# Kernel tuning notes

Measured on AMD Instinct MI355X. Metric: run time of the kernel, lower is better.

## Reference

```python
import jax, jax.numpy as jnp
import numpy as np

N = 3072        # seeds = 3 * batch (src, dst, neg)
K = 64          # num_tokens (sampled neighbors per seed)
C = 128         # edge_dim (mixer channels)
T = 100         # time_dim
ND = 128        # node_dim
ED = 128        # embed_dim
NUM_NODES = 100000
TG = 98304      # total flattened time-gap neighbor indices
L = 2           # num mixer layers
TH = int(K * 0.5)   # token hidden = 32
CH = int(C * 4.0)   # channel hidden = 512
PAD = 0         # PADDED_NODE_ID


def setup_inputs() -> dict:
    key = jax.random.key(0)
    ks = jax.random.split(key, 32)
    inp = {}
    inp['edge_feat'] = jax.random.normal(ks[0], (N, K, C), jnp.float32)
    inp['seed_times'] = jax.random.uniform(ks[1], (N,), jnp.float32) * 1000.0
    inp['nbr_time'] = jax.random.uniform(ks[2], (N, K), jnp.float32) * 1000.0
    inp['node_feat'] = jax.random.normal(ks[3], (NUM_NODES, ND), jnp.float32)
    # Time2Vec frozen frequencies (GraphMixer style)
    inp['time_w'] = jnp.asarray(1.0 / np.power(10.0, np.linspace(0.0, 9.0, T)), jnp.float32)
    s = 0.02
    inp['proj_W'] = jax.random.normal(ks[4], (C + T, C), jnp.float32) * s
    inp['proj_b'] = jnp.zeros((C,), jnp.float32)
    inp['ln1_g'] = jnp.ones((L, C), jnp.float32)
    inp['ln1_b'] = jnp.zeros((L, C), jnp.float32)
    inp['tW1'] = jax.random.normal(ks[5], (L, K, TH), jnp.float32) * s
    inp['tb1'] = jnp.zeros((L, TH), jnp.float32)
    inp['tW2'] = jax.random.normal(ks[6], (L, TH, K), jnp.float32) * s
    inp['tb2'] = jnp.zeros((L, K), jnp.float32)
    inp['ln2_g'] = jnp.ones((L, C), jnp.float32)
    inp['ln2_b'] = jnp.zeros((L, C), jnp.float32)
    inp['cW1'] = jax.random.normal(ks[7], (L, C, CH), jnp.float32) * s
    inp['cb1'] = jnp.zeros((L, CH), jnp.float32)
    inp['cW2'] = jax.random.normal(ks[8], (L, CH, C), jnp.float32) * s
    inp['cb2'] = jnp.zeros((L, C), jnp.float32)
    inp['out_W'] = jax.random.normal(ks[9], (C + ND, ED), jnp.float32) * s
    inp['out_b'] = jnp.zeros((ED,), jnp.float32)
    inp['nbr_nids'] = jax.random.randint(ks[10], (N, K), 0, NUM_NODES, jnp.int32)
    inp['tg_idx'] = jax.random.randint(ks[11], (TG,), 0, NUM_NODES, jnp.int32)
    inp['tg_seg'] = jnp.sort(jax.random.randint(ks[12], (TG,), 0, N, jnp.int32))
    inp['seed_ids'] = jax.random.randint(ks[13], (N,), 0, NUM_NODES, jnp.int32)
    return inp


def _ln(x, g, b):
    m = jnp.mean(x, axis=-1, keepdims=True)
    v = jnp.var(x, axis=-1, keepdims=True)
    return (x - m) * jax.lax.rsqrt(v + 1e-5) * g + b


def reference(edge_feat, seed_times, nbr_time, node_feat, time_w, proj_W, proj_b,
              ln1_g, ln1_b, tW1, tb1, tW2, tb2, ln2_g, ln2_b, cW1, cb1, cW2, cb2,
              out_W, out_b, nbr_nids, tg_idx, tg_seg, seed_ids):
    # Time2Vec on time deltas: [N, K, T]
    dt = seed_times[:, None] - nbr_time
    tfeat = jnp.cos(dt[..., None] * time_w)
    # projection: [N, K, C]
    z = jnp.concatenate([edge_feat, tfeat], axis=-1) @ proj_W + proj_b
    # MLP-Mixer layers (token mixing over K, channel mixing over C)
    for l in range(L):
        h = _ln(z, ln1_g[l], ln1_b[l])
        h = jnp.einsum('nkc,kh->nhc', h, tW1[l]) + tb1[l][None, :, None]
        h = jax.nn.gelu(h)
        h = jnp.einsum('nhc,hk->nkc', h, tW2[l]) + tb2[l][None, :, None]
        z = z + h
        h = _ln(z, ln2_g[l], ln2_b[l])
        h = jax.nn.gelu(h @ cW1[l] + cb1[l]) @ cW2[l] + cb2[l]
        z = z + h
    # masked mean over valid neighbors -> [N, C]
    mask = (nbr_nids != PAD).astype(z.dtype)
    z = jnp.sum(z * mask[..., None], axis=1) / jnp.clip(jnp.sum(mask, axis=1, keepdims=True), 1.0)
    # ragged segment-mean over time-gap neighbors (replaces Python loop)
    counts = jax.ops.segment_sum(jnp.ones((TG,), z.dtype), tg_seg, num_segments=N)
    tg_feat = jax.ops.segment_sum(node_feat[tg_idx], tg_seg, num_segments=N) / jnp.clip(counts, 1.0)[:, None]
    z_node = tg_feat + node_feat[seed_ids]
    return jnp.concatenate([z, z_node], axis=1) @ out_W + out_b
```

## Files before the change

### kernel.cpp

```cpp
#include <hip/hip_runtime.h>
#include <math.h>

#define NS   3072
#define KT   64
#define CC   128
#define TDIM 100
#define TGN  98304
#define TH   32
#define CH   512
#define ZS   132
#define PS   136
#define PS2  264
#define PSK  72
#define PSH  40

typedef __attribute__((ext_vector_type(8))) short bf16x8;
typedef __attribute__((ext_vector_type(4))) float f32x4;

__device__ __forceinline__ unsigned short f2bf(float f) {
    unsigned int u = __float_as_uint(f);
    return (unsigned short)((u + 0x7FFFu + ((u >> 16) & 1u)) >> 16);
}
__device__ __forceinline__ float fast_exp2(float x) {
    float r; asm("v_exp_f32 %0, %1" : "=v"(r) : "v"(x)); return r;
}
__device__ __forceinline__ float fast_rcp(float x) {
    float r; asm("v_rcp_f32 %0, %1" : "=v"(r) : "v"(x)); return r;
}
__device__ __forceinline__ float fast_cos2pi(float rev) {
    float f = rev - floorf(rev);
    float r; asm("v_cos_f32 %0, %1" : "=v"(r) : "v"(f)); return r;
}
__device__ __forceinline__ unsigned int pk_bf16(float lo, float hi) {
    unsigned int r; asm("v_cvt_pk_bf16_f32 %0, %1, %2" : "=v"(r) : "v"(lo), "v"(hi)); return r;
}
__device__ __forceinline__ float gelu_f(float x) {
    float p = x * x;
    float e = fast_exp2(-x * fmaf(p, 0.1029436f, 2.3022082f));
    return x * fast_rcp(1.0f + e);
}

__global__ void gm_prep(const float* __restrict__ proj_W, const float* __restrict__ tW1,
                        const float* __restrict__ tW2, const float* __restrict__ cW1,
                        const float* __restrict__ cW2,
                        unsigned short* __restrict__ projWTb, unsigned short* __restrict__ tW1Tb,
                        unsigned short* __restrict__ tW2Tb, unsigned short* __restrict__ cW1Tb,
                        unsigned short* __restrict__ cW2Tb)
{
    int e = blockIdx.x * 256 + threadIdx.x;
    if (e < 32768) {
        int c = e >> 8, j = e & 255;
        projWTb[e] = (j < 228) ? f2bf(proj_W[j * CC + c]) : (unsigned short)0;
    }
    int e1 = e - 32768;
    if (e1 >= 0 && e1 < 4096) {
        int l = e1 >> 11, rem = e1 & 2047, h = rem >> 6, k = rem & 63;
        tW1Tb[e1] = f2bf(tW1[(l * KT + k) * TH + h]);
    }
    int e2 = e - 36864;
    if (e2 >= 0 && e2 < 4096) {
        int l = e2 >> 11, rem = e2 & 2047, k = rem >> 5, h = rem & 31;
        tW2Tb[e2] = f2bf(tW2[(l * TH + h) * KT + k]);
    }
    int e3 = e - 40960;
    if (e3 >= 0 && e3 < 131072) {
        int l = e3 >> 16, rem = e3 & 65535, h = rem >> 7, c = rem & 127;
        cW1Tb[e3] = f2bf(cW1[(l * CC + c) * CH + h]);
    }
    int e4 = e - 172032;
    if (e4 >= 0 && e4 < 131072) {
        int l = e4 >> 16, rem = e4 & 65535, c = rem >> 9, h = rem & 511;
        cW2Tb[e4] = f2bf(cW2[(l * CH + h) * CC + c]);
    }
}

__global__ __launch_bounds__(256, 2)
void gm_mixer(const float* __restrict__ edge_feat,
              const float* __restrict__ seed_times,
              const float* __restrict__ nbr_time,
              const float* __restrict__ time_w,
              const float* __restrict__ proj_b,
              const float* __restrict__ ln1_g, const float* __restrict__ ln1_b,
              const float* __restrict__ tb1,   const float* __restrict__ tb2,
              const float* __restrict__ ln2_g, const float* __restrict__ ln2_b,
              const float* __restrict__ cb1,   const float* __restrict__ cb2,
              const int*   __restrict__ nbr_nids,
              const unsigned short* __restrict__ projWTb,
              const unsigned short* __restrict__ tW1Tb,
              const unsigned short* __restrict__ tW2Tb,
              const unsigned short* __restrict__ cW1Tb,
              const unsigned short* __restrict__ cW2Tb,
              float* __restrict__ zmean)
{
    __shared__ float zbuf[KT * ZS];
    __shared__ short ubuf[17408];
    __shared__ float mArr[KT], rArr[KT], maskArr[KT];

    const int n  = blockIdx.x;
    const int t  = threadIdx.x;
    const int w  = t >> 6;
    const int l  = t & 63;
    const int lr = l & 15;
    const int kg = l >> 4;

    const f32x4 zero4 = {0.f, 0.f, 0.f, 0.f};

    short* Ab = ubuf;
    if (t < KT) {
        mArr[t]    = seed_times[n] - nbr_time[n * KT + t];
        maskArr[t] = (nbr_nids[n * KT + t] != 0) ? 1.0f : 0.0f;
    }
    {
        const float4* ef4 = (const float4*)(edge_feat + (size_t)n * KT * CC);
        #pragma unroll
        for (int it = 0; it < 8; ++it) {
            int i4 = it * 256 + t;
            int k  = i4 >> 5;
            int c  = (i4 & 31) << 2;
            float4 v = ef4[i4];
            uint2 pk;
            pk.x = pk_bf16(v.x, v.y);
            pk.y = pk_bf16(v.z, v.w);
            *(uint2*)&Ab[k * PS2 + c] = pk;
        }
    }
    __syncthreads();
    for (int idx = t; idx < 4096; idx += 256) {
        int k = idx >> 6, j2 = (idx & 63) << 1;
        unsigned int pack = 0;
        if (j2 < TDIM) {
            float dt = mArr[k];
            float2 twv = *(const float2*)&time_w[j2];
            float v0 = fast_cos2pi(dt * twv.x * 0.15915494309f);
            float v1 = fast_cos2pi(dt * twv.y * 0.15915494309f);
            pack = pk_bf16(v0, v1);
        }
        *(unsigned int*)&Ab[k * PS2 + 128 + j2] = pack;
    }
    __syncthreads();

    {
        f32x4 acc[4][2];
        #pragma unroll
        for (int mt = 0; mt < 4; ++mt) { acc[mt][0] = zero4; acc[mt][1] = zero4; }
        for (int ks = 0; ks < 8; ++ks) {
            bf16x8 b0 = *(const bf16x8*)&projWTb[(w * 32 + lr)      * 256 + ks * 32 + kg * 8];
            bf16x8 b1 = *(const bf16x8*)&projWTb[(w * 32 + 16 + lr) * 256 + ks * 32 + kg * 8];
            #pragma unroll
            for (int mt = 0; mt < 4; ++mt) {
                bf16x8 a = *(const bf16x8*)&Ab[(mt * 16 + lr) * PS2 + ks * 32 + kg * 8];
                acc[mt][0] = __builtin_amdgcn_mfma_f32_16x16x32_bf16(a, b0, acc[mt][0], 0, 0, 0);
                acc[mt][1] = __builtin_amdgcn_mfma_f32_16x16x32_bf16(a, b1, acc[mt][1], 0, 0, 0);
            }
        }
        __syncthreads();
        #pragma unroll
        for (int mt = 0; mt < 4; ++mt)
            #pragma unroll
            for (int nt = 0; nt < 2; ++nt) {
                int col = w * 32 + nt * 16 + lr;
                float pb = proj_b[col];
                #pragma unroll
                for (int r = 0; r < 4; ++r)
                    zbuf[(mt * 16 + kg * 4 + r) * ZS + col] = acc[mt][nt][r] + pb;
            }
    }
    __syncthreads();

    short* LNz1T = ubuf;
    short* G2T   = ubuf + 128 * PSK;
    short* LNzb  = ubuf;
    short* Gb    = ubuf + 64 * PS;

    for (int lay = 0; lay < 2; ++lay) {
        {
            int rr = t >> 2, part = t & 3;
            const float4* zp = (const float4*)&zbuf[rr * ZS + part * 32];
            float s = 0.f, s2 = 0.f;
            #pragma unroll
            for (int i = 0; i < 8; ++i) {
                float4 v = zp[i];
                s  += v.x + v.y + v.z + v.w;
                s2 += v.x * v.x + v.y * v.y + v.z * v.z + v.w * v.w;
            }
            s += __shfl_xor(s, 1); s2 += __shfl_xor(s2, 1);
            s += __shfl_xor(s, 2); s2 += __shfl_xor(s2, 2);
            if (part == 0) {
                float m = s * (1.0f / CC);
                float var = s2 * (1.0f / CC) - m * m;
                mArr[rr] = m; rArr[rr] = rsqrtf(var + 1e-5f);
            }
        }
        __syncthreads();

        {
            const float* g1 = ln1_g + lay * CC;
            const float* b1 = ln1_b + lay * CC;
            const int kk = l;
            const float mk = mArr[kk], rk = rArr[kk];
            #pragma unroll
            for (int it = 0; it < 16; ++it) {
                int c = w * 2 + it * 8;
                float2 zv = *(const float2*)&zbuf[kk * ZS + c];
                float v0 = (zv.x - mk) * rk * g1[c]     + b1[c];
                float v1 = (zv.y - mk) * rk * g1[c + 1] + b1[c + 1];
                unsigned int pk = pk_bf16(v0, v1);
                LNz1T[c * PSK + kk]       = (short)(pk & 0xFFFFu);
                LNz1T[(c + 1) * PSK + kk] = (short)(pk >> 16);
            }
        }
        __syncthreads();

        {
            f32x4 acc1[2][2];
            #pragma unroll
            for (int mt = 0; mt < 2; ++mt) { acc1[mt][0] = zero4; acc1[mt][1] = zero4; }
            #pragma unroll
            for (int ks = 0; ks < 2; ++ks) {
                bf16x8 bb0 = *(const bf16x8*)&LNz1T[(w * 32 + lr)      * PSK + ks * 32 + kg * 8];
                bf16x8 bb1 = *(const bf16x8*)&LNz1T[(w * 32 + 16 + lr) * PSK + ks * 32 + kg * 8];
                #pragma unroll
                for (int mt = 0; mt < 2; ++mt) {
                    bf16x8 a = *(const bf16x8*)&tW1Tb[lay * 2048 + (mt * 16 + lr) * 64 + ks * 32 + kg * 8];
                    acc1[mt][0] = __builtin_amdgcn_mfma_f32_16x16x32_bf16(a, bb0, acc1[mt][0], 0, 0, 0);
                    acc1[mt][1] = __builtin_amdgcn_mfma_f32_16x16x32_bf16(a, bb1, acc1[mt][1], 0, 0, 0);
                }
            }
            #pragma unroll
            for (int mt = 0; mt < 2; ++mt) {
                float4 tbv = *(const float4*)&tb1[lay * TH + mt * 16 + kg * 4];
                #pragma unroll
                for (int nt = 0; nt < 2; ++nt) {
                    int col = w * 32 + nt * 16 + lr;
                    float g0 = gelu_f(acc1[mt][nt][0] + tbv.x);
                    float g1v = gelu_f(acc1[mt][nt][1] + tbv.y);
                    float g2 = gelu_f(acc1[mt][nt][2] + tbv.z);
                    float g3 = gelu_f(acc1[mt][nt][3] + tbv.w);
                    uint2 pk;
                    pk.x = pk_bf16(g0, g1v);
                    pk.y = pk_bf16(g2, g3);
                    *(uint2*)&G2T[col * PSH + mt * 16 + kg * 4] = pk;
                }
            }
        }
        {
            f32x4 acc2[4][2];
            #pragma unroll
            for (int mt = 0; mt < 4; ++mt) { acc2[mt][0] = zero4; acc2[mt][1] = zero4; }
            bf16x8 bb0 = *(const bf16x8*)&G2T[(w * 32 + lr)      * PSH + kg * 8];
            bf16x8 bb1 = *(const bf16x8*)&G2T[(w * 32 + 16 + lr) * PSH + kg * 8];
            #pragma unroll
            for (int mt = 0; mt < 4; ++mt) {
                bf16x8 a = *(const bf16x8*)&tW2Tb[lay * 2048 + (mt * 16 + lr) * 32 + kg * 8];
                acc2[mt][0] = __builtin_amdgcn_mfma_f32_16x16x32_bf16(a, bb0, acc2[mt][0], 0, 0, 0);
                acc2[mt][1] = __builtin_amdgcn_mfma_f32_16x16x32_bf16(a, bb1, acc2[mt][1], 0, 0, 0);
            }
            #pragma unroll
            for (int mt = 0; mt < 4; ++mt)
                #pragma unroll
                for (int nt = 0; nt < 2; ++nt) {
                    int col = w * 32 + nt * 16 + lr;
                    #pragma unroll
                    for (int r = 0; r < 4; ++r) {
                        int row = mt * 16 + kg * 4 + r;
                        zbuf[row * ZS + col] += acc2[mt][nt][r] + tb2[lay * KT + row];
                    }
                }
        }
        __syncthreads();

        {
            int rr = t >> 2, part = t & 3;
            const float4* zp = (const float4*)&zbuf[rr * ZS + part * 32];
            float s = 0.f, s2 = 0.f;
            #pragma unroll
            for (int i = 0; i < 8; ++i) {
                float4 v = zp[i];
                s  += v.x + v.y + v.z + v.w;
                s2 += v.x * v.x + v.y * v.y + v.z * v.z + v.w * v.w;
            }
            s += __shfl_xor(s, 1); s2 += __shfl_xor(s2, 1);
            s += __shfl_xor(s, 2); s2 += __shfl_xor(s2, 2);
            if (part == 0) {
                float m = s * (1.0f / CC);
                float var = s2 * (1.0f / CC) - m * m;
                mArr[rr] = m; rArr[rr] = rsqrtf(var + 1e-5f);
            }
        }
        __syncthreads();

        {
            const float* g2 = ln2_g + lay * CC;
            const float* b2 = ln2_b + lay * CC;
            for (int idx = t; idx < 4096; idx += 256) {
                int k = idx >> 6, c2 = (idx & 63) << 1;
                float m = mArr[k], r = rArr[k];
                float v0 = (zbuf[k * ZS + c2]     - m) * r * g2[c2]     + b2[c2];
                float v1 = (zbuf[k * ZS + c2 + 1] - m) * r * g2[c2 + 1] + b2[c2 + 1];
                *(unsigned int*)&LNzb[k * PS + c2] = pk_bf16(v0, v1);
            }
        }
        __syncthreads();

        {
            f32x4 accB[4][2];
            #pragma unroll
            for (int mt = 0; mt < 4; ++mt) { accB[mt][0] = zero4; accB[mt][1] = zero4; }

            for (int jc = 0; jc < 4; ++jc) {
                f32x4 accA[4][2];
                #pragma unroll
                for (int mt = 0; mt < 4; ++mt) { accA[mt][0] = zero4; accA[mt][1] = zero4; }
                #pragma unroll
                for (int ks = 0; ks < 4; ++ks) {
                    const unsigned short* w1p = cW1Tb + lay * CH * CC
                                              + (jc * 128 + w * 32 + lr) * CC + ks * 32 + kg * 8;
                    bf16x8 a0 = *(const bf16x8*)w1p;
                    bf16x8 a1 = *(const bf16x8*)(w1p + 16 * CC);
                    #pragma unroll
                    for (int mt = 0; mt < 4; ++mt) {
                        bf16x8 b = *(const bf16x8*)&LNzb[(mt * 16 + lr) * PS + ks * 32 + kg * 8];
                        accA[mt][0] = __builtin_amdgcn_mfma_f32_16x16x32_bf16(a0, b, accA[mt][0], 0, 0, 0);
                        accA[mt][1] = __builtin_amdgcn_mfma_f32_16x16x32_bf16(a1, b, accA[mt][1], 0, 0, 0);
                    }
                }
                #pragma unroll
                for (int nt = 0; nt < 2; ++nt) {
                    int j0 = w * 32 + nt * 16 + kg * 4;
                    float4 cbv = *(const float4*)&cb1[lay * CH + jc * 128 + j0];
                    #pragma unroll
                    for (int mt = 0; mt < 4; ++mt) {
                        float g0 = gelu_f(accA[mt][nt][0] + cbv.x);
                        float g1v = gelu_f(accA[mt][nt][1] + cbv.y);
                        float g2 = gelu_f(accA[mt][nt][2] + cbv.z);
                        float g3 = gelu_f(accA[mt][nt][3] + cbv.w);
                        uint2 pk;
                        pk.x = pk_bf16(g0, g1v);
                        pk.y = pk_bf16(g2, g3);
                        *(uint2*)&Gb[(mt * 16 + lr) * PS + j0] = pk;
                    }
                }
                __syncthreads();
                #pragma unroll
                for (int ks = 0; ks < 4; ++ks) {
                    const unsigned short* w2p = cW2Tb + lay * CC * CH
                                              + (w * 32 + lr) * CH + jc * 128 + ks * 32 + kg * 8;
                    bf16x8 b0 = *(const bf16x8*)w2p;
                    bf16x8 b1 = *(const bf16x8*)(w2p + 16 * CH);
                    #pragma unroll
                    for (int mt = 0; mt < 4; ++mt) {
                        bf16x8 a = *(const bf16x8*)&Gb[(mt * 16 + lr) * PS + ks * 32 + kg * 8];
                        accB[mt][0] = __builtin_amdgcn_mfma_f32_16x16x32_bf16(a, b0, accB[mt][0], 0, 0, 0);
                        accB[mt][1] = __builtin_amdgcn_mfma_f32_16x16x32_bf16(a, b1, accB[mt][1], 0, 0, 0);
                    }
                }
                __syncthreads();
            }
            #pragma unroll
            for (int mt = 0; mt < 4; ++mt)
                #pragma unroll
                for (int nt = 0; nt < 2; ++nt) {
                    int col = w * 32 + nt * 16 + lr;
                    float cb = cb2[lay * CC + col];
                    #pragma unroll
                    for (int r = 0; r < 4; ++r)
                        zbuf[(mt * 16 + kg * 4 + r) * ZS + col] += accB[mt][nt][r] + cb;
                }
        }
        __syncthreads();
    }

    {
        float* red = (float*)ubuf;
        const int c = t & 127, h = t >> 7;
        float acc = 0.f, ms = 0.f;
        for (int k = h * 32; k < h * 32 + 32; ++k) {
            float mk = maskArr[k];
            ms  += mk;
            acc += zbuf[k * ZS + c] * mk;
        }
        red[h * 128 + c] = acc;
        red[256 + h * 128 + c] = ms;
        __syncthreads();
        if (t < CC) {
            float tot  = red[t] + red[128 + t];
            float mtot = red[256 + t] + red[384 + t];
            zmean[n * CC + t] = tot / fmaxf(mtot, 1.0f);
        }
    }
}

__global__ __launch_bounds__(256)
void gm_out(const float* __restrict__ zmean,
            const float* __restrict__ node_feat,
            const float* __restrict__ out_W,
            const float* __restrict__ out_b,
            const int*   __restrict__ tg_idx,
            const int*   __restrict__ tg_seg,
            const int*   __restrict__ seed_ids,
            float* __restrict__ outp)
{
    __shared__ float redf[8 * 132];
    __shared__ float zmL[CC], znL[CC], oL[2 * CC];
    const int n = blockIdx.x;
    const int t = threadIdx.x;
    const int q = t & 31, g = t >> 5;

    int a = 0, b = TGN;
    while (a < b) { int mm = (a + b) >> 1; if (tg_seg[mm] < n) a = mm + 1; else b = mm; }
    const int lo = a;
    int a2 = lo, b2 = TGN;
    while (a2 < b2) { int mm = (a2 + b2) >> 1; if (tg_seg[mm] < n + 1) a2 = mm + 1; else b2 = mm; }
    const int hi = a2;

    float4 acc = {0.f, 0.f, 0.f, 0.f};
    for (int i = lo + g; i < hi; i += 8) {
        int nid = tg_idx[i];
        const float4* nf = (const float4*)(node_feat + (size_t)nid * CC);
        float4 v = nf[q];
        acc.x += v.x; acc.y += v.y; acc.z += v.z; acc.w += v.w;
    }
    *(float4*)&redf[g * 132 + q * 4] = acc;
    __syncthreads();
    if (t < CC) {
        float s = 0.f;
        #pragma unroll
        for (int gg = 0; gg < 8; ++gg) s += redf[gg * 132 + t];
        float cnt = (float)(hi - lo);
        znL[t] = s / fmaxf(cnt, 1.0f) + node_feat[(size_t)seed_ids[n] * CC + t];
        zmL[t] = zmean[n * CC + t];
    }
    __syncthreads();
    {
        const int c = t & 127, h = t >> 7;
        const float* src = h ? znL : zmL;
        const float* Wp  = out_W + (size_t)h * CC * 128;
        float o = 0.f;
        for (int j = 0; j < CC; ++j) o += src[j] * Wp[j * 128 + c];
        oL[h * 128 + c] = o;
    }
    __syncthreads();
    if (t < CC) outp[n * 128 + t] = oL[t] + oL[CC + t] + out_b[t];
}

extern "C" void kernel_launch(void* const* d_in, const int* in_sizes, int n_in,
                              void* d_out, int out_size, void* d_ws, size_t ws_size,
                              hipStream_t stream)
{
    const float* edge_feat  = (const float*)d_in[0];
    const float* seed_times = (const float*)d_in[1];
    const float* nbr_time   = (const float*)d_in[2];
    const float* node_feat  = (const float*)d_in[3];
    const float* time_w     = (const float*)d_in[4];
    const float* proj_W     = (const float*)d_in[5];
    const float* proj_b     = (const float*)d_in[6];
    const float* ln1_g      = (const float*)d_in[7];
    const float* ln1_b      = (const float*)d_in[8];
    const float* tW1        = (const float*)d_in[9];
    const float* tb1        = (const float*)d_in[10];
    const float* tW2        = (const float*)d_in[11];
    const float* tb2        = (const float*)d_in[12];
    const float* ln2_g      = (const float*)d_in[13];
    const float* ln2_b      = (const float*)d_in[14];
    const float* cW1        = (const float*)d_in[15];
    const float* cb1        = (const float*)d_in[16];
    const float* cW2        = (const float*)d_in[17];
    const float* cb2        = (const float*)d_in[18];
    const float* out_W      = (const float*)d_in[19];
    const float* out_b      = (const float*)d_in[20];
    const int*   nbr_nids   = (const int*)d_in[21];
    const int*   tg_idx     = (const int*)d_in[22];
    const int*   tg_seg     = (const int*)d_in[23];
    const int*   seed_ids   = (const int*)d_in[24];

    char* ws = (char*)d_ws;
    float*          zmean   = (float*)ws;
    unsigned short* projWTb = (unsigned short*)(ws + 1572864);
    unsigned short* tW1Tb   = (unsigned short*)(ws + 1638400);
    unsigned short* tW2Tb   = (unsigned short*)(ws + 1646592);
    unsigned short* cW1Tb   = (unsigned short*)(ws + 1654784);
    unsigned short* cW2Tb   = (unsigned short*)(ws + 1916928);

    gm_prep<<<1184, 256, 0, stream>>>(proj_W, tW1, tW2, cW1, cW2,
                                      projWTb, tW1Tb, tW2Tb, cW1Tb, cW2Tb);
    gm_mixer<<<NS, 256, 0, stream>>>(edge_feat, seed_times, nbr_time, time_w,
                                     proj_b, ln1_g, ln1_b, tb1, tb2, ln2_g, ln2_b,
                                     cb1, cb2, nbr_nids,
                                     projWTb, tW1Tb, tW2Tb, cW1Tb, cW2Tb, zmean);
    gm_out<<<NS, 256, 0, stream>>>(zmean, node_feat, out_W, out_b,
                                   tg_idx, tg_seg, seed_ids, (float*)d_out);
}
```

Baseline: 571.0 us.

## Keep mixer residual stream in registers and drop fp32 LDS z buffer

The residual activation z now stays in MFMA accumulator registers across both mixer layers instead of an fp32 shared-memory buffer. LayerNorm statistics come from cross-lane shuffles plus a small per-wave partial-sum array, and the masked mean reduces in registers. With the large LDS buffer gone, the launch bound rises to three blocks per CU, and the projection GEMM is split into two passes so the time features reuse the edge-feature staging area. Weight preparation becomes tiled LDS transposes for coalesced access; more live registers may cause spills under the tighter occupancy bound.

```diff
diff --git a/kernel.cpp b/kernel.cpp
--- a/kernel.cpp
+++ b/kernel.cpp
@@ -8,9 +8,8 @@
 #define TGN  98304
 #define TH   32
 #define CH   512
-#define ZS   132
 #define PS   136
-#define PS2  264
+#define PSA  136
 #define PSK  72
 #define PSH  40
 
@@ -40,41 +39,57 @@
     return x * fast_rcp(1.0f + e);
 }
 
-__global__ void gm_prep(const float* __restrict__ proj_W, const float* __restrict__ tW1,
-                        const float* __restrict__ tW2, const float* __restrict__ cW1,
-                        const float* __restrict__ cW2,
-                        unsigned short* __restrict__ projWTb, unsigned short* __restrict__ tW1Tb,
-                        unsigned short* __restrict__ tW2Tb, unsigned short* __restrict__ cW1Tb,
-                        unsigned short* __restrict__ cW2Tb)
+__global__ __launch_bounds__(256)
+void gm_trans(const float* __restrict__ cW1, const float* __restrict__ cW2,
+              const float* __restrict__ proj_W,
+              unsigned short* __restrict__ cW1Tb, unsigned short* __restrict__ cW2Tb,
+              unsigned short* __restrict__ projWTb)
+{
+    __shared__ float tile[32][33];
+    const int bid = blockIdx.x;
+    const float* src; unsigned short* dst;
+    int R, Cs, oC, tr, tc;
+    if (bid < 128) {
+        int l = bid >> 6, q = bid & 63; tr = q >> 4; tc = q & 15;
+        src = cW1 + l * CC * CH; dst = cW1Tb + l * CH * CC; R = CC; Cs = CH; oC = CC;
+    } else if (bid < 256) {
+        int b = bid - 128, l = b >> 6, q = b & 63; tr = q & 15; tc = q >> 4;
+        src = cW2 + l * CH * CC; dst = cW2Tb + l * CC * CH; R = CH; Cs = CC; oC = CH;
+    } else {
+        int b = bid - 256; tr = b >> 2; tc = b & 3;
+        src = proj_W; dst = projWTb; R = 228; Cs = CC; oC = 256;
+    }
+    const int tx = threadIdx.x & 31, ty0 = threadIdx.x >> 5;
+    #pragma unroll
+    for (int i = 0; i < 4; ++i) {
+        int ty = ty0 + i * 8;
+        int rr = tr * 32 + ty, cc = tc * 32 + tx;
+        tile[ty][tx] = (rr < R) ? src[rr * Cs + cc] : 0.0f;
+    }
+    __syncthreads();
+    #pragma unroll
+    for (int i = 0; i < 4; ++i) {
+        int ty = ty0 + i * 8;
+        int orow = tc * 32 + ty, ocol = tr * 32 + tx;
+        dst[orow * oC + ocol] = f2bf(tile[tx][ty]);
+    }
+}
+
+__global__ __launch_bounds__(256)
+void gm_prep_small(const float* __restrict__ tW1, const float* __restrict__ tW2,
+                   unsigned short* __restrict__ tW1Tb, unsigned short* __restrict__ tW2Tb)
 {
     int e = blockIdx.x * 256 + threadIdx.x;
-    if (e < 32768) {
-        int c = e >> 8, j = e & 255;
-        projWTb[e] = (j < 228) ? f2bf(proj_W[j * CC + c]) : (unsigned short)0;
-    }
-    int e1 = e - 32768;
-    if (e1 >= 0 && e1 < 4096) {
-        int l = e1 >> 11, rem = e1 & 2047, h = rem >> 6, k = rem & 63;
-        tW1Tb[e1] = f2bf(tW1[(l * KT + k) * TH + h]);
-    }
-    int e2 = e - 36864;
-    if (e2 >= 0 && e2 < 4096) {
-        int l = e2 >> 11, rem = e2 & 2047, k = rem >> 5, h = rem & 31;
+    if (e < 4096) {
+        int l = e >> 11, rem = e & 2047, h = rem >> 6, k = rem & 63;
+        tW1Tb[e] = f2bf(tW1[(l * KT + k) * TH + h]);
+    } else {
+        int e2 = e - 4096, l = e2 >> 11, rem = e2 & 2047, k = rem >> 5, h = rem & 31;
         tW2Tb[e2] = f2bf(tW2[(l * TH + h) * KT + k]);
     }
-    int e3 = e - 40960;
-    if (e3 >= 0 && e3 < 131072) {
-        int l = e3 >> 16, rem = e3 & 65535, h = rem >> 7, c = rem & 127;
-        cW1Tb[e3] = f2bf(cW1[(l * CC + c) * CH + h]);
-    }
-    int e4 = e - 172032;
-    if (e4 >= 0 && e4 < 131072) {
-        int l = e4 >> 16, rem = e4 & 65535, c = rem >> 9, h = rem & 511;
-        cW2Tb[e4] = f2bf(cW2[(l * CH + h) * CC + c]);
-    }
-}
-
-__global__ __launch_bounds__(256, 2)
+}
+
+__global__ __launch_bounds__(256, 3)
 void gm_mixer(const float* __restrict__ edge_feat,
               const float* __restrict__ seed_times,
               const float* __restrict__ nbr_time,
@@ -92,9 +107,9 @@
               const unsigned short* __restrict__ cW2Tb,
               float* __restrict__ zmean)
 {
-    __shared__ float zbuf[KT * ZS];
     __shared__ short ubuf[17408];
-    __shared__ float mArr[KT], rArr[KT], maskArr[KT];
+    __shared__ float lnS[256], lnS2[256];
+    __shared__ float mArr[KT], rArr[KT], maskArr[KT], dtArr[KT];
 
     const int n  = blockIdx.x;
     const int t  = threadIdx.x;
@@ -102,114 +117,134 @@
     const int l  = t & 63;
     const int lr = l & 15;
     const int kg = l >> 4;
-
-    const f32x4 zero4 = {0.f, 0.f, 0.f, 0.f};
-
-    short* Ab = ubuf;
-    if (t < KT) {
-        mArr[t]    = seed_times[n] - nbr_time[n * KT + t];
-        maskArr[t] = (nbr_nids[n * KT + t] != 0) ? 1.0f : 0.0f;
-    }
-    {
-        const float4* ef4 = (const float4*)(edge_feat + (size_t)n * KT * CC);
-        #pragma unroll
-        for (int it = 0; it < 8; ++it) {
-            int i4 = it * 256 + t;
-            int k  = i4 >> 5;
-            int c  = (i4 & 31) << 2;
-            float4 v = ef4[i4];
-            uint2 pk;
-            pk.x = pk_bf16(v.x, v.y);
-            pk.y = pk_bf16(v.z, v.w);
-            *(uint2*)&Ab[k * PS2 + c] = pk;
-        }
-    }
-    __syncthreads();
-    for (int idx = t; idx < 4096; idx += 256) {
-        int k = idx >> 6, j2 = (idx & 63) << 1;
-        unsigned int pack = 0;
-        if (j2 < TDIM) {
-            float dt = mArr[k];
-            float2 twv = *(const float2*)&time_w[j2];
-            float v0 = fast_cos2pi(dt * twv.x * 0.15915494309f);
-            float v1 = fast_cos2pi(dt * twv.y * 0.15915494309f);
-            pack = pk_bf16(v0, v1);
-        }
-        *(unsigned int*)&Ab[k * PS2 + 128 + j2] = pack;
-    }
-    __syncthreads();
-
-    {
-        f32x4 acc[4][2];
-        #pragma unroll
-        for (int mt = 0; mt < 4; ++mt) { acc[mt][0] = zero4; acc[mt][1] = zero4; }
-        for (int ks = 0; ks < 8; ++ks) {
-            bf16x8 b0 = *(const bf16x8*)&projWTb[(w * 32 + lr)      * 256 + ks * 32 + kg * 8];
-            bf16x8 b1 = *(const bf16x8*)&projWTb[(w * 32 + 16 + lr) * 256 + ks * 32 + kg * 8];
-            #pragma unroll
-            for (int mt = 0; mt < 4; ++mt) {
-                bf16x8 a = *(const bf16x8*)&Ab[(mt * 16 + lr) * PS2 + ks * 32 + kg * 8];
-                acc[mt][0] = __builtin_amdgcn_mfma_f32_16x16x32_bf16(a, b0, acc[mt][0], 0, 0, 0);
-                acc[mt][1] = __builtin_amdgcn_mfma_f32_16x16x32_bf16(a, b1, acc[mt][1], 0, 0, 0);
-            }
-        }
-        __syncthreads();
-        #pragma unroll
-        for (int mt = 0; mt < 4; ++mt)
-            #pragma unroll
-            for (int nt = 0; nt < 2; ++nt) {
-                int col = w * 32 + nt * 16 + lr;
-                float pb = proj_b[col];
-                #pragma unroll
-                for (int r = 0; r < 4; ++r)
-                    zbuf[(mt * 16 + kg * 4 + r) * ZS + col] = acc[mt][nt][r] + pb;
-            }
-    }
-    __syncthreads();
-
+    const int c0 = w * 32 + lr;
+    const int c1 = c0 + 16;
+
+    short* Ab    = ubuf;
     short* LNz1T = ubuf;
     short* G2T   = ubuf + 128 * PSK;
     short* LNzb  = ubuf;
     short* Gb    = ubuf + 64 * PS;
 
+    const f32x4 zero4 = {0.f, 0.f, 0.f, 0.f};
+    f32x4 zr[4][2];
+
+    if (t < KT) {
+        dtArr[t]   = seed_times[n] - nbr_time[n * KT + t];
+        maskArr[t] = (nbr_nids[n * KT + t] != 0) ? 1.0f : 0.0f;
+    }
+    {
+        const float4* ef4 = (const float4*)(edge_feat + (size_t)n * KT * CC);
+        #pragma unroll
+        for (int it = 0; it < 8; ++it) {
+            int i4 = it * 256 + t;
+            int k = i4 >> 5, c = (i4 & 31) << 2;
+            float4 v = ef4[i4];
+            uint2 pk; pk.x = pk_bf16(v.x, v.y); pk.y = pk_bf16(v.z, v.w);
+            *(uint2*)&Ab[k * PSA + c] = pk;
+        }
+    }
+    __syncthreads();
+
+    {
+        f32x4 acc[4][2];
+        #pragma unroll
+        for (int mt = 0; mt < 4; ++mt) { acc[mt][0] = zero4; acc[mt][1] = zero4; }
+        #pragma unroll
+        for (int p = 0; p < 2; ++p) {
+            #pragma unroll
+            for (int ks = 0; ks < 4; ++ks) {
+                const unsigned short* bp = projWTb + (w * 32 + lr) * 256 + p * 128 + ks * 32 + kg * 8;
+                bf16x8 b0 = *(const bf16x8*)bp;
+                bf16x8 b1 = *(const bf16x8*)(bp + 16 * 256);
+                #pragma unroll
+                for (int mt = 0; mt < 4; ++mt) {
+                    bf16x8 a = *(const bf16x8*)&Ab[(mt * 16 + lr) * PSA + ks * 32 + kg * 8];
+                    acc[mt][0] = __builtin_amdgcn_mfma_f32_16x16x32_bf16(a, b0, acc[mt][0], 0, 0, 0);
+                    acc[mt][1] = __builtin_amdgcn_mfma_f32_16x16x32_bf16(a, b1, acc[mt][1], 0, 0, 0);
+                }
+            }
+            if (p == 0) {
+                __syncthreads();
+                #pragma unroll
+                for (int it = 0; it < 16; ++it) {
+                    int idx = it * 256 + t;
+                    int k = idx >> 6, j2 = (idx & 63) << 1;
+                    unsigned pk = 0;
+                    if (j2 < TDIM) {
+                        float dt = dtArr[k];
+                        float2 twv = *(const float2*)&time_w[j2];
+                        pk = pk_bf16(fast_cos2pi(dt * twv.x * 0.15915494309f),
+                                     fast_cos2pi(dt * twv.y * 0.15915494309f));
+                    }
+                    *(unsigned*)&Ab[k * PSA + j2] = pk;
+                }
+                __syncthreads();
+            }
+        }
+        #pragma unroll
+        for (int mt = 0; mt < 4; ++mt)
+            #pragma unroll
+            for (int nt = 0; nt < 2; ++nt) {
+                float pb = proj_b[nt ? c1 : c0];
+                #pragma unroll
+                for (int r = 0; r < 4; ++r) zr[mt][nt][r] = acc[mt][nt][r] + pb;
+            }
+    }
+
     for (int lay = 0; lay < 2; ++lay) {
-        {
-            int rr = t >> 2, part = t & 3;
-            const float4* zp = (const float4*)&zbuf[rr * ZS + part * 32];
-            float s = 0.f, s2 = 0.f;
-            #pragma unroll
-            for (int i = 0; i < 8; ++i) {
-                float4 v = zp[i];
-                s  += v.x + v.y + v.z + v.w;
-                s2 += v.x * v.x + v.y * v.y + v.z * v.z + v.w * v.w;
-            }
-            s += __shfl_xor(s, 1); s2 += __shfl_xor(s2, 1);
-            s += __shfl_xor(s, 2); s2 += __shfl_xor(s2, 2);
-            if (part == 0) {
-                float m = s * (1.0f / CC);
-                float var = s2 * (1.0f / CC) - m * m;
-                mArr[rr] = m; rArr[rr] = rsqrtf(var + 1e-5f);
-            }
+        #pragma unroll
+        for (int mt = 0; mt < 4; ++mt) {
+            f32x4 sv, qv;
+            #pragma unroll
+            for (int r = 0; r < 4; ++r) {
+                float z0 = zr[mt][0][r], z1 = zr[mt][1][r];
+                sv[r] = z0 + z1;
+                qv[r] = z0 * z0 + z1 * z1;
+            }
+            #pragma unroll
+            for (int d = 1; d < 16; d <<= 1)
+                #pragma unroll
+                for (int r = 0; r < 4; ++r) {
+                    sv[r] += __shfl_xor(sv[r], d);
+                    qv[r] += __shfl_xor(qv[r], d);
+                }
+            if (lr == 0) {
+                *(f32x4*)&lnS [w * 64 + mt * 16 + kg * 4] = sv;
+                *(f32x4*)&lnS2[w * 64 + mt * 16 + kg * 4] = qv;
+            }
+        }
+        __syncthreads();
+        if (t < KT) {
+            float s  = lnS [t] + lnS [64 + t] + lnS [128 + t] + lnS [192 + t];
+            float s2 = lnS2[t] + lnS2[64 + t] + lnS2[128 + t] + lnS2[192 + t];
+            float m = s * (1.0f / CC);
+            float var = s2 * (1.0f / CC) - m * m;
+            mArr[t] = m; rArr[t] = rsqrtf(var + 1e-5f);
         }
         __syncthreads();
 
         {
             const float* g1 = ln1_g + lay * CC;
             const float* b1 = ln1_b + lay * CC;
-            const int kk = l;
-            const float mk = mArr[kk], rk = rArr[kk];
-            #pragma unroll
-            for (int it = 0; it < 16; ++it) {
-                int c = w * 2 + it * 8;
-                float2 zv = *(const float2*)&zbuf[kk * ZS + c];
-                float v0 = (zv.x - mk) * rk * g1[c]     + b1[c];
-                float v1 = (zv.y - mk) * rk * g1[c + 1] + b1[c + 1];
-                unsigned int pk = pk_bf16(v0, v1);
-                LNz1T[c * PSK + kk]       = (short)(pk & 0xFFFFu);
-                LNz1T[(c + 1) * PSK + kk] = (short)(pk >> 16);
-            }
-        }
-        __syncthreads();
+            float gc0 = g1[c0], bc0 = b1[c0], gc1 = g1[c1], bc1 = b1[c1];
+            #pragma unroll
+            for (int mt = 0; mt < 4; ++mt) {
+                f32x4 mv = *(const f32x4*)&mArr[mt * 16 + kg * 4];
+                f32x4 rv = *(const f32x4*)&rArr[mt * 16 + kg * 4];
+                #pragma unroll
+                for (int nt = 0; nt < 2; ++nt) {
+                    float gg = nt ? gc1 : gc0, bb = nt ? bc1 : bc0;
+                    int c = nt ? c1 : c0;
+                    float v0 = (zr[mt][nt][0] - mv[0]) * rv[0] * gg + bb;
+                    float v1 = (zr[mt][nt][1] - mv[1]) * rv[1] * gg + bb;
+                    float v2 = (zr[mt][nt][2] - mv[2]) * rv[2] * gg + bb;
+                    float v3 = (zr[mt][nt][3] - mv[3]) * rv[3] * gg + bb;
+                    uint2 pk; pk.x = pk_bf16(v0, v1); pk.y = pk_bf16(v2, v3);
+                    *(uint2*)&LNz1T[c * PSK + mt * 16 + kg * 4] = pk;
+                }
+            }
+        }
 
         {
             f32x4 acc1[2][2];
@@ -217,8 +252,8 @@
             for (int mt = 0; mt < 2; ++mt) { acc1[mt][0] = zero4; acc1[mt][1] = zero4; }
             #pragma unroll
             for (int ks = 0; ks < 2; ++ks) {
-                bf16x8 bb0 = *(const bf16x8*)&LNz1T[(w * 32 + lr)      * PSK + ks * 32 + kg * 8];
-                bf16x8 bb1 = *(const bf16x8*)&LNz1T[(w * 32 + 16 + lr) * PSK + ks * 32 + kg * 8];
+                bf16x8 bb0 = *(const bf16x8*)&LNz1T[c0 * PSK + ks * 32 + kg * 8];
+                bf16x8 bb1 = *(const bf16x8*)&LNz1T[c1 * PSK + ks * 32 + kg * 8];
                 #pragma unroll
                 for (int mt = 0; mt < 2; ++mt) {
                     bf16x8 a = *(const bf16x8*)&tW1Tb[lay * 2048 + (mt * 16 + lr) * 64 + ks * 32 + kg * 8];
@@ -231,73 +266,87 @@
                 float4 tbv = *(const float4*)&tb1[lay * TH + mt * 16 + kg * 4];
                 #pragma unroll
                 for (int nt = 0; nt < 2; ++nt) {
-                    int col = w * 32 + nt * 16 + lr;
+                    int c = nt ? c1 : c0;
                     float g0 = gelu_f(acc1[mt][nt][0] + tbv.x);
                     float g1v = gelu_f(acc1[mt][nt][1] + tbv.y);
                     float g2 = gelu_f(acc1[mt][nt][2] + tbv.z);
                     float g3 = gelu_f(acc1[mt][nt][3] + tbv.w);
-                    uint2 pk;
-                    pk.x = pk_bf16(g0, g1v);
-                    pk.y = pk_bf16(g2, g3);
-                    *(uint2*)&G2T[col * PSH + mt * 16 + kg * 4] = pk;
+                    uint2 pk; pk.x = pk_bf16(g0, g1v); pk.y = pk_bf16(g2, g3);
+                    *(uint2*)&G2T[c * PSH + mt * 16 + kg * 4] = pk;
                 }
             }
         }
         {
-            f32x4 acc2[4][2];
-            #pragma unroll
-            for (int mt = 0; mt < 4; ++mt) { acc2[mt][0] = zero4; acc2[mt][1] = zero4; }
-            bf16x8 bb0 = *(const bf16x8*)&G2T[(w * 32 + lr)      * PSH + kg * 8];
-            bf16x8 bb1 = *(const bf16x8*)&G2T[(w * 32 + 16 + lr) * PSH + kg * 8];
+            bf16x8 bb0 = *(const bf16x8*)&G2T[c0 * PSH + kg * 8];
+            bf16x8 bb1 = *(const bf16x8*)&G2T[c1 * PSH + kg * 8];
             #pragma unroll
             for (int mt = 0; mt < 4; ++mt) {
+                f32x4 a2v0 = zero4, a2v1 = zero4;
                 bf16x8 a = *(const bf16x8*)&tW2Tb[lay * 2048 + (mt * 16 + lr) * 32 + kg * 8];
-                acc2[mt][0] = __builtin_amdgcn_mfma_f32_16x16x32_bf16(a, bb0, acc2[mt][0], 0, 0, 0);
-                acc2[mt][1] = __builtin_amdgcn_mfma_f32_16x16x32_bf16(a, bb1, acc2[mt][1], 0, 0, 0);
-            }
-            #pragma unroll
-            for (int mt = 0; mt < 4; ++mt)
-                #pragma unroll
-                for (int nt = 0; nt < 2; ++nt) {
-                    int col = w * 32 + nt * 16 + lr;
-                    #pragma unroll
-                    for (int r = 0; r < 4; ++r) {
-                        int row = mt * 16 + kg * 4 + r;
-                        zbuf[row * ZS + col] += acc2[mt][nt][r] + tb2[lay * KT + row];
-                    }
-                }
+                a2v0 = __builtin_amdgcn_mfma_f32_16x16x32_bf16(a, bb0, a2v0, 0, 0, 0);
+                a2v1 = __builtin_amdgcn_mfma_f32_16x16x32_bf16(a, bb1, a2v1, 0, 0, 0);
+                float4 t2v = *(const float4*)&tb2[lay * KT + mt * 16 + kg * 4];
+                #pragma unroll
+                for (int r = 0; r < 4; ++r) {
+                    float tb = (r == 0) ? t2v.x : (r == 1) ? t2v.y : (r == 2) ? t2v.z : t2v.w;
+                    zr[mt][0][r] += a2v0[r] + tb;
+                    zr[mt][1][r] += a2v1[r] + tb;
+                }
+            }
+        }
+
+        #pragma unroll
+        for (int mt = 0; mt < 4; ++mt) {
+            f32x4 sv, qv;
+            #pragma unroll
+            for (int r = 0; r < 4; ++r) {
+                float z0 = zr[mt][0][r], z1 = zr[mt][1][r];
+                sv[r] = z0 + z1;
+                qv[r] = z0 * z0 + z1 * z1;
+            }
+            #pragma unroll
+            for (int d = 1; d < 16; d <<= 1)
+                #pragma unroll
+                for (int r = 0; r < 4; ++r) {
+                    sv[r] += __shfl_xor(sv[r], d);
+                    qv[r] += __shfl_xor(qv[r], d);
+                }
+            if (lr == 0) {
+                *(f32x4*)&lnS [w * 64 + mt * 16 + kg * 4] = sv;
+                *(f32x4*)&lnS2[w * 64 + mt * 16 + kg * 4] = qv;
+            }
         }
         __syncthreads();
-
-        {
-            int rr = t >> 2, part = t & 3;
-            const float4* zp = (const float4*)&zbuf[rr * ZS + part * 32];
-            float s = 0.f, s2 = 0.f;
-            #pragma unroll
-            for (int i = 0; i < 8; ++i) {
-                float4 v = zp[i];
-                s  += v.x + v.y + v.z + v.w;
-                s2 += v.x * v.x + v.y * v.y + v.z * v.z + v.w * v.w;
-            }
-            s += __shfl_xor(s, 1); s2 += __shfl_xor(s2, 1);
-            s += __shfl_xor(s, 2); s2 += __shfl_xor(s2, 2);
-            if (part == 0) {
-                float m = s * (1.0f / CC);
-                float var = s2 * (1.0f / CC) - m * m;
-                mArr[rr] = m; rArr[rr] = rsqrtf(var + 1e-5f);
-            }
+        if (t < KT) {
+            float s  = lnS [t] + lnS [64 + t] + lnS [128 + t] + lnS [192 + t];
+            float s2 = lnS2[t] + lnS2[64 + t] + lnS2[128 + t] + lnS2[192 + t];
+            float m = s * (1.0f / CC);
+            float var = s2 * (1.0f / CC) - m * m;
+            mArr[t] = m; rArr[t] = rsqrtf(var + 1e-5f);
         }
         __syncthreads();
 
         {
             const float* g2 = ln2_g + lay * CC;
             const float* b2 = ln2_b + lay * CC;
-            for (int idx = t; idx < 4096; idx += 256) {
-                int k = idx >> 6, c2 = (idx & 63) << 1;
-                float m = mArr[k], r = rArr[k];
-                float v0 = (zbuf[k * ZS + c2]     - m) * r * g2[c2]     + b2[c2];
-                float v1 = (zbuf[k * ZS + c2 + 1] - m) * r * g2[c2 + 1] + b2[c2 + 1];
-                *(unsigned int*)&LNzb[k * PS + c2] = pk_bf16(v0, v1);
+            float gc0 = g2[c0], bc0 = b2[c0], gc1 = g2[c1], bc1 = b2[c1];
+            const bool odd = lr & 1;
+            const int cb = odd ? (c1 - 1) : c0;
+            #pragma unroll
+            for (int mt = 0; mt < 4; ++mt) {
+                f32x4 mv = *(const f32x4*)&mArr[mt * 16 + kg * 4];
+                f32x4 rv = *(const f32x4*)&rArr[mt * 16 + kg * 4];
+                #pragma unroll
+                for (int r = 0; r < 4; ++r) {
+                    float v0 = (zr[mt][0][r] - mv[r]) * rv[r] * gc0 + bc0;
+                    float v1 = (zr[mt][1][r] - mv[r]) * rv[r] * gc1 + bc1;
+                    float s0 = __shfl_xor(v0, 1);
+                    float s1 = __shfl_xor(v1, 1);
+                    unsigned pka = pk_bf16(v0, s0);
+                    unsigned pkb = pk_bf16(s1, v1);
+                    unsigned pkv = odd ? pkb : pka;
+                    *(unsigned*)&LNzb[(mt * 16 + kg * 4 + r) * PS + cb] = pkv;
+                }
             }
         }
         __syncthreads();
@@ -334,9 +383,7 @@
                         float g1v = gelu_f(accA[mt][nt][1] + cbv.y);
                         float g2 = gelu_f(accA[mt][nt][2] + cbv.z);
                         float g3 = gelu_f(accA[mt][nt][3] + cbv.w);
-                        uint2 pk;
-                        pk.x = pk_bf16(g0, g1v);
-                        pk.y = pk_bf16(g2, g3);
+                        uint2 pk; pk.x = pk_bf16(g0, g1v); pk.y = pk_bf16(g2, g3);
                         *(uint2*)&Gb[(mt * 16 + lr) * PS + j0] = pk;
                     }
                 }
@@ -360,32 +407,32 @@
             for (int mt = 0; mt < 4; ++mt)
                 #pragma unroll
                 for (int nt = 0; nt < 2; ++nt) {
-                    int col = w * 32 + nt * 16 + lr;
-                    float cb = cb2[lay * CC + col];
+                    float cb = cb2[lay * CC + (nt ? c1 : c0)];
                     #pragma unroll
-                    for (int r = 0; r < 4; ++r)
-                        zbuf[(mt * 16 + kg * 4 + r) * ZS + col] += accB[mt][nt][r] + cb;
-                }
-        }
-        __syncthreads();
+                    for (int r = 0; r < 4; ++r) zr[mt][nt][r] += accB[mt][nt][r] + cb;
+                }
+        }
     }
 
     {
-        float* red = (float*)ubuf;
-        const int c = t & 127, h = t >> 7;
-        float acc = 0.f, ms = 0.f;
-        for (int k = h * 32; k < h * 32 + 32; ++k) {
-            float mk = maskArr[k];
-            ms  += mk;
-            acc += zbuf[k * ZS + c] * mk;
-        }
-        red[h * 128 + c] = acc;
-        red[256 + h * 128 + c] = ms;
-        __syncthreads();
-        if (t < CC) {
-            float tot  = red[t] + red[128 + t];
-            float mtot = red[256 + t] + red[384 + t];
-            zmean[n * CC + t] = tot / fmaxf(mtot, 1.0f);
+        float msum = 0.f, a0v = 0.f, a1v = 0.f;
+        #pragma unroll
+        for (int mt = 0; mt < 4; ++mt) {
+            f32x4 mk4 = *(const f32x4*)&maskArr[mt * 16 + kg * 4];
+            #pragma unroll
+            for (int r = 0; r < 4; ++r) {
+                msum += mk4[r];
+                a0v  += zr[mt][0][r] * mk4[r];
+                a1v  += zr[mt][1][r] * mk4[r];
+            }
+        }
+        a0v  += __shfl_xor(a0v, 16);  a0v  += __shfl_xor(a0v, 32);
+        a1v  += __shfl_xor(a1v, 16);  a1v  += __shfl_xor(a1v, 32);
+        msum += __shfl_xor(msum, 16); msum += __shfl_xor(msum, 32);
+        if (kg == 0) {
+            float inv = fast_rcp(fmaxf(msum, 1.0f));
+            zmean[n * CC + c0] = a0v * inv;
+            zmean[n * CC + c1] = a1v * inv;
         }
     }
 }
@@ -481,8 +528,8 @@
     unsigned short* cW1Tb   = (unsigned short*)(ws + 1654784);
     unsigned short* cW2Tb   = (unsigned short*)(ws + 1916928);
 
-    gm_prep<<<1184, 256, 0, stream>>>(proj_W, tW1, tW2, cW1, cW2,
-                                      projWTb, tW1Tb, tW2Tb, cW1Tb, cW2Tb);
+    gm_trans<<<288, 256, 0, stream>>>(cW1, cW2, proj_W, cW1Tb, cW2Tb, projWTb);
+    gm_prep_small<<<32, 256, 0, stream>>>(tW1, tW2, tW1Tb, tW2Tb);
     gm_mixer<<<NS, 256, 0, stream>>>(edge_feat, seed_times, nbr_time, time_w,
                                      proj_b, ln1_g, ln1_b, tb1, tb2, ln2_g, ln2_b,
                                      cb1, cb2, nbr_nids,
```

New measurement: 524.0 us. 8.2% less time.
